# Kernel tuning notes

Measured on AMD Instinct MI355X. Metric: run time of the kernel, lower is better.

The kernel has to match this reference:

```python
import jax, jax.numpy as jnp
import numpy as np

N_NODES = 100000
N_EDGES = 1600000
D_IN = 128
D_H = 128
NUM_GRAPHS = 128


def setup_inputs() -> dict:
    key = jax.random.key(0)
    ks = jax.random.split(key, 16)
    x = jax.random.normal(ks[0], (N_NODES, D_IN), dtype=jnp.float32)
    edge_index = jax.random.randint(ks[1], (2, N_EDGES), 0, N_NODES, dtype=jnp.int64)
    batch_index = jnp.sort(jax.random.randint(ks[2], (N_NODES,), 0, NUM_GRAPHS, dtype=jnp.int64))
    s = 0.05
    W1 = s * jax.random.normal(ks[3], (D_IN, D_H), dtype=jnp.float32)
    b1 = jnp.zeros((D_H,), jnp.float32)
    W2 = s * jax.random.normal(ks[4], (D_H, D_H), dtype=jnp.float32)
    b2 = jnp.zeros((D_H,), jnp.float32)
    W3 = s * jax.random.normal(ks[5], (D_H, D_H), dtype=jnp.float32)
    b3 = jnp.zeros((D_H,), jnp.float32)
    W4 = s * jax.random.normal(ks[6], (D_H, D_H), dtype=jnp.float32)
    b4 = jnp.zeros((D_H,), jnp.float32)
    Wl = s * jax.random.normal(ks[7], (2 * D_H, 1), dtype=jnp.float32)
    bl = jnp.zeros((1,), jnp.float32)
    return {"x": x, "edge_index": edge_index, "batch_index": batch_index,
            "W1": W1, "b1": b1, "W2": W2, "b2": b2, "W3": W3, "b3": b3,
            "W4": W4, "b4": b4, "Wl": Wl, "bl": bl}


def _gcn_prep(edge_index, n_nodes):
    # add self-loops, symmetric normalization D^-1/2 (A+I) D^-1/2
    loops = jnp.arange(n_nodes, dtype=edge_index.dtype)
    row = jnp.concatenate([edge_index[0], loops])  # source
    col = jnp.concatenate([edge_index[1], loops])  # target
    deg = jax.ops.segment_sum(jnp.ones_like(col, dtype=jnp.float32), col,
                              num_segments=n_nodes)
    dinv = jnp.where(deg > 0, jax.lax.rsqrt(jnp.maximum(deg, 1.0)), 0.0)
    norm = dinv[row] * dinv[col]  # [E+N]
    return row, col, norm


def _gcn(h, W, b, row, col, norm, n_nodes):
    h = h @ W                                   # [N, H]
    msg = h[row] * norm[:, None]                # gather + scale
    return jax.ops.segment_sum(msg, col, num_segments=n_nodes) + b


def reference(x, edge_index, batch_index, W1, b1, W2, b2, W3, b3, W4, b4, Wl, bl):
    n = x.shape[0]
    row, col, norm = _gcn_prep(edge_index, n)
    h = jnp.tanh(_gcn(x, W1, b1, row, col, norm, n))
    h = jnp.tanh(_gcn(h, W2, b2, row, col, norm, n))
    h = jnp.tanh(_gcn(h, W3, b3, row, col, norm, n))
    h = jnp.tanh(_gcn(h, W4, b4, row, col, norm, n))
    # global max / mean pool per graph
    cnt = jax.ops.segment_sum(jnp.ones((n,), jnp.float32), batch_index,
                              num_segments=NUM_GRAPHS)
    mx = jax.ops.segment_max(h, batch_index, num_segments=NUM_GRAPHS)
    mx = jnp.where(cnt[:, None] > 0, mx, 0.0)
    sm = jax.ops.segment_sum(h, batch_index, num_segments=NUM_GRAPHS)
    mn = sm / jnp.maximum(cnt, 1.0)[:, None]
    pooled = jnp.concatenate([mx, mn], axis=1)  # [G, 2H]
    return pooled @ Wl + bl                     # [G, 1]
```

## Files before the change

### kernel.cpp

```cpp
#include <hip/hip_runtime.h>
#include <hip/hip_bf16.h>
#include <math.h>

#define PSPLIT 8
#define BSH 8
#define NBMAX 512
#define CHUNK 8192
#define AST 40

typedef float v4f __attribute__((ext_vector_type(4)));
typedef float v2f __attribute__((ext_vector_type(2)));
typedef unsigned int v4u __attribute__((ext_vector_type(4)));
typedef unsigned int v2u __attribute__((ext_vector_type(2)));
typedef __attribute__((ext_vector_type(8))) short bf8;
typedef __attribute__((ext_vector_type(4))) float f4;
typedef unsigned short u16;
typedef unsigned int u32;

static inline size_t align_up(size_t x, size_t a){ return (x + a - 1) & ~(a - 1); }

__device__ inline void bf_split(float v, u16& hi, u16& lo){
  __hip_bfloat16 h = __float2bfloat16(v);
  float hf = __bfloat162float(h);
  __hip_bfloat16 l = __float2bfloat16(v - hf);
  hi = *(u16*)&h; lo = *(u16*)&l;
}

__device__ inline void fmixlo(float& a, u32 p){
  asm("v_fma_mix_f32 %0, %1, 1.0, %0 op_sel:[0,0,0] op_sel_hi:[1,0,0]" : "+v"(a) : "v"(p));
}
__device__ inline void fmixhi(float& a, u32 p){
  asm("v_fma_mix_f32 %0, %1, 1.0, %0 op_sel:[1,0,0] op_sel_hi:[1,0,0]" : "+v"(a) : "v"(p));
}

__device__ inline float tanh_fast(float x){
  float u = __builtin_amdgcn_exp2f(x * 2.8853900817779268f);
  float q = __builtin_amdgcn_rcpf(u + 1.0f);
  return fmaf(-2.0f, q, 1.0f);
}


__global__ __launch_bounds__(256) void k_bhist(const int* __restrict__ col, int* __restrict__ bcnt,
                                               int E, int NB,
                                               const int* __restrict__ batch, int* __restrict__ gstart,
                                               int n, int G){
  extern __shared__ int lh[];
  for (int i = threadIdx.x; i < NB; i += 256) lh[i] = 0;
  __syncthreads();
  for (int e = blockIdx.x * 256 + threadIdx.x; e < E; e += gridDim.x * 256)
    atomicAdd(&lh[col[e] >> BSH], 1);
  __syncthreads();
  for (int i = threadIdx.x; i < NB; i += 256){
    int v = lh[i];
    if (v) atomicAdd(&bcnt[i], v);
  }
  for (int i = blockIdx.x * 256 + threadIdx.x; i < n; i += gridDim.x * 256){
    int cb = batch[i];
    if (i == 0){ for (int g = 0; g <= cb; ++g) gstart[g] = 0; }
    else { int pb = batch[i - 1]; for (int g = pb + 1; g <= cb; ++g) gstart[g] = i; }
    if (i == n - 1){ for (int g = cb + 1; g <= G; ++g) gstart[g] = n; }
  }
}

__global__ void k_bscan(const int* __restrict__ bcnt, int* __restrict__ boff, int NB, int E,
                        int* __restrict__ rp, int N){
  __shared__ int sd[256];
  int t = threadIdx.x;
  int c[16]; int s = 0;
  const int PT = (NB + 255) / 256;
  for (int j = 0; j < PT; ++j){ int i = t * PT + j; c[j] = (i < NB) ? bcnt[i] : 0; s += c[j]; }
  sd[t] = s; __syncthreads();
  for (int off = 1; off < 256; off <<= 1){
    int v = sd[t];
    if (t >= off) v += sd[t - off];
    __syncthreads(); sd[t] = v; __syncthreads();
  }
  int run = sd[t] - s;
  for (int j = 0; j < PT; ++j){ int i = t * PT + j; if (i < NB) boff[i] = run; run += c[j]; }
  if (t == 255){ boff[NB] = run; rp[N] = E; }
}

__global__ __launch_bounds__(256) void k_bscat(const int* __restrict__ ei, const int* __restrict__ boff,
                                               int* __restrict__ bfill, unsigned* __restrict__ tmp,
                                               int E, int NB){
  __shared__ int lh[NBMAX], loff[NBMAX], gb[NBMAX], lfil[NBMAX];
  __shared__ int sd[256];
  __shared__ int sumA;
  __shared__ u32 stg[CHUNK];
  int t = threadIdx.x;
  const int* col = ei + E;
  int c0 = blockIdx.x * CHUNK;
  int c1 = c0 + CHUNK; if (c1 > E) c1 = E;

  for (int i = t; i < NBMAX; i += 256){ lh[i] = 0; lfil[i] = 0; }
  __syncthreads();
  for (int e = c0 + t; e < c1; e += 256)
    atomicAdd(&lh[col[e] >> BSH], 1);
  __syncthreads();
  sd[t] = lh[t]; __syncthreads();
  for (int off = 1; off < 256; off <<= 1){
    int v = sd[t];
    if (t >= off) v += sd[t - off];
    __syncthreads(); sd[t] = v; __syncthreads();
  }
  loff[t] = sd[t] - lh[t];
  if (t == 255) sumA = sd[255];
  __syncthreads();
  int lb = lh[256 + t];
  sd[t] = lb; __syncthreads();
  for (int off = 1; off < 256; off <<= 1){
    int v = sd[t];
    if (t >= off) v += sd[t - off];
    __syncthreads(); sd[t] = v; __syncthreads();
  }
  loff[256 + t] = sumA + sd[t] - lb;
  for (int i = t; i < NB; i += 256){
    int c = lh[i];
    gb[i] = c ? (boff[i] + atomicAdd(&bfill[i * 16], c)) : 0;
  }
  __syncthreads();
  for (int e = c0 + t; e < c1; e += 256){
    int d = col[e], s = ei[e];
    int b = d >> BSH;
    int p = atomicAdd(&lfil[b], 1);
    stg[loff[b] + p] = (unsigned)s | ((unsigned)(d & 255) << 17);
  }
  __syncthreads();
  int wv = t >> 6, lane = t & 63;
  for (int b = wv; b < NB; b += 4){
    int len = lh[b];
    if (!len) continue;
    int base = gb[b], lo = loff[b];
    for (int j = lane; j < len; j += 64) tmp[base + j] = stg[lo + j];
  }
}

__global__ __launch_bounds__(256) void k_bfin(const unsigned* __restrict__ tmp, const int* __restrict__ boff,
                                              int* __restrict__ ssrc, int* __restrict__ rp,
                                              float* __restrict__ dinv, int N){
  int b = blockIdx.x;
  int d0 = b << BSH;
  int lim = N - d0; if (lim > 256) lim = 256;
  __shared__ int dcnt[256], dexc[256], lfill[256];
  int t = threadIdx.x;
  dcnt[t] = 0; lfill[t] = 0;
  __syncthreads();
  int lo = boff[b], hi = boff[b + 1];
  for (int i = lo + t; i < hi; i += 256) atomicAdd(&dcnt[tmp[i] >> 17], 1);
  __syncthreads();
  int cme = dcnt[t];
  dexc[t] = cme; __syncthreads();
  for (int off = 1; off < 256; off <<= 1){
    int v = dexc[t];
    if (t >= off) v += dexc[t - off];
    __syncthreads(); dexc[t] = v; __syncthreads();
  }
  int excl = dexc[t] - cme;
  __syncthreads();
  dexc[t] = excl;
  if (t < lim){
    int d = d0 + t;
    rp[d] = lo + excl;
    double dd = (double)(cme + 1);
    dinv[d] = (float)(1.0 / sqrt(dd));
  }
  __syncthreads();
  for (int i = lo + t; i < hi; i += 256){
    unsigned r = tmp[i];
    int l = r >> 17;
    int pos = dexc[l] + atomicAdd(&lfill[l], 1);
    ssrc[lo + pos] = (int)(r & 0x1FFFFu);
  }
}


__global__ __launch_bounds__(256) void k_cvtw(const float* __restrict__ w0, const float* __restrict__ w1,
                                              const float* __restrict__ w2, const float* __restrict__ w3,
                                              u16* __restrict__ wth, u16* __restrict__ wtl){
  int id = blockIdx.x * 256 + threadIdx.x;
  if (id >= 4 * 16384) return;
  int l = id >> 14, rem = id & 16383, k = rem >> 7, nn = rem & 127;
  const float* Wsrc = (l == 0) ? w0 : (l == 1) ? w1 : (l == 2) ? w2 : w3;
  float v = Wsrc[k * 128 + nn];
  u16 hi, lo; bf_split(v, hi, lo);
  wth[(l << 14) + nn * 128 + k] = hi;
  wtl[(l << 14) + nn * 128 + k] = lo;
}


__global__ __launch_bounds__(256, 4) void k_gemm(const float* __restrict__ A,
                                                 const u16* __restrict__ wth, const u16* __restrict__ wtl,
                                                 const float* __restrict__ dinv,
                                                 u16* __restrict__ C, int n, int packed){
  __shared__ u16 Ah[128 * AST], Al[128 * AST], Wh[128 * AST], Wl[128 * AST];
  int t = threadIdx.x;
  int r0 = blockIdx.x * 128;
  int wv = t >> 6, lane = t & 63;
  int q = lane >> 4, ln = lane & 15;

  int srow = t >> 1;
  int shalf = (t & 1) * 16;
  int grow = r0 + srow; if (grow > n - 1) grow = n - 1;
  const float* ga = A + (size_t)grow * 128 + shalf;
  const u16* gwh = wth + srow * 128 + shalf;
  const u16* gwl = wtl + srow * 128 + shalf;

  f4 acc[2][8];
  #pragma unroll
  for (int mt = 0; mt < 2; ++mt)
    #pragma unroll
    for (int nt = 0; nt < 8; ++nt) acc[mt][nt] = (f4)(0.f);

  for (int c = 0; c < 4; ++c){
    __syncthreads();
    {
      u16* ah = &Ah[srow * AST + shalf];
      u16* al = &Al[srow * AST + shalf];
      if (packed){
        const v4u* gp = (const v4u*)(ga + c * 32);
        #pragma unroll
        for (int i = 0; i < 4; ++i){
          v4u v = gp[i];
          ushort4 hv = {(u16)(v.x >> 16), (u16)(v.y >> 16), (u16)(v.z >> 16), (u16)(v.w >> 16)};
          ushort4 lv = {(u16)v.x, (u16)v.y, (u16)v.z, (u16)v.w};
          *(ushort4*)&ah[i * 4] = hv;
          *(ushort4*)&al[i * 4] = lv;
        }
      } else {
        const float4* gp = (const float4*)(ga + c * 32);
        #pragma unroll
        for (int i = 0; i < 4; ++i){
          float4 v = gp[i];
          u16 h0,h1,h2,h3,l0,l1,l2,l3;
          bf_split(v.x, h0, l0); bf_split(v.y, h1, l1);
          bf_split(v.z, h2, l2); bf_split(v.w, h3, l3);
          ushort4 hv = {h0,h1,h2,h3}, lv = {l0,l1,l2,l3};
          *(ushort4*)&ah[i * 4] = hv;
          *(ushort4*)&al[i * 4] = lv;
        }
      }
    }
    {
      const u16* ph = gwh + c * 32;
      const u16* pl = gwl + c * 32;
      bf8 h0 = *(const bf8*)ph, h1 = *(const bf8*)(ph + 8);
      bf8 l0 = *(const bf8*)pl, l1 = *(const bf8*)(pl + 8);
      *(bf8*)&Wh[srow * AST + shalf] = h0; *(bf8*)&Wh[srow * AST + shalf + 8] = h1;
      *(bf8*)&Wl[srow * AST + shalf] = l0; *(bf8*)&Wl[srow * AST + shalf + 8] = l1;
    }
    __syncthreads();

    bf8 afh[2], afl[2];
    #pragma unroll
    for (int mt = 0; mt < 2; ++mt){
      int row = wv * 32 + mt * 16 + ln;
      afh[mt] = *(const bf8*)&Ah[row * AST + q * 8];
      afl[mt] = *(const bf8*)&Al[row * AST + q * 8];
    }
    #pragma unroll
    for (int nt = 0; nt < 8; ++nt){
      int wn = nt * 16 + ln;
      bf8 wfh = *(const bf8*)&Wh[wn * AST + q * 8];
      bf8 wfl = *(const bf8*)&Wl[wn * AST + q * 8];
      #pragma unroll
      for (int mt = 0; mt < 2; ++mt){
        acc[mt][nt] = __builtin_amdgcn_mfma_f32_16x16x32_bf16(afh[mt], wfh, acc[mt][nt], 0, 0, 0);
        acc[mt][nt] = __builtin_amdgcn_mfma_f32_16x16x32_bf16(afl[mt], wfh, acc[mt][nt], 0, 0, 0);
        acc[mt][nt] = __builtin_amdgcn_mfma_f32_16x16x32_bf16(afh[mt], wfl, acc[mt][nt], 0, 0, 0);
      }
    }
  }

  #pragma unroll
  for (int mt = 0; mt < 2; ++mt){
    int base_m = r0 + wv * 32 + mt * 16 + q * 4;
    float dv[4];
    #pragma unroll
    for (int reg = 0; reg < 4; ++reg){
      int row = base_m + reg;
      dv[reg] = (row < n) ? dinv[row] : 0.f;
    }
    #pragma unroll
    for (int nt = 0; nt < 8; ++nt){
      #pragma unroll
      for (int reg = 0; reg < 4; ++reg){
        int row = base_m + reg;
        if (row < n){
          _Float16 hv = (_Float16)(acc[mt][nt][reg] * dv[reg]);
          C[(size_t)row * 128 + nt * 16 + ln] = *(u16*)&hv;
        }
      }
    }
  }
}


__global__ __launch_bounds__(256) void k_agg(const u16* __restrict__ hwp, const int* __restrict__ rp,
                                             const int* __restrict__ ssrc,
                                             const float* __restrict__ dinv, const float* __restrict__ bias,
                                             float* __restrict__ hout, int n, int pack){
  int node = blockIdx.x * 4 + (threadIdx.x >> 6);
  node = __builtin_amdgcn_readfirstlane(node);
  if (node >= n) return;
  int lane = threadIdx.x & 63;
  const u32* hw32 = (const u32*)hwp;

  int e0 = rp[node], e1 = rp[node + 1];
  float a0 = 0.f, a1 = 0.f;
  int e = e0;
  while (e + 16 <= e1){
    u32 p[16];
    #pragma unroll
    for (int i = 0; i < 16; ++i){
      int s = ssrc[e + i];
      p[i] = hw32[(size_t)s * 64 + lane];
    }
    #pragma unroll
    for (int i = 0; i < 16; ++i){ fmixlo(a0, p[i]); fmixhi(a1, p[i]); }
    e += 16;
  }
  while (e + 4 <= e1){
    u32 p[4];
    #pragma unroll
    for (int i = 0; i < 4; ++i){
      int s = ssrc[e + i];
      p[i] = hw32[(size_t)s * 64 + lane];
    }
    #pragma unroll
    for (int i = 0; i < 4; ++i){ fmixlo(a0, p[i]); fmixhi(a1, p[i]); }
    e += 4;
  }
  while (e < e1){
    int s = ssrc[e];
    u32 p = hw32[(size_t)s * 64 + lane];
    fmixlo(a0, p); fmixhi(a1, p);
    ++e;
  }
  {
    u32 p = hw32[(size_t)node * 64 + lane];
    fmixlo(a0, p); fmixhi(a1, p);
  }
  float di = dinv[node];
  v2f bv = *(const v2f*)(bias + lane * 2);
  float r0 = tanh_fast(fmaf(a0, di, bv.x));
  float r1 = tanh_fast(fmaf(a1, di, bv.y));
  if (pack){
    u16 h0, h1, l0, l1;
    bf_split(r0, h0, l0); bf_split(r1, h1, l1);
    v2u pv;
    pv.x = ((u32)h0 << 16) | l0;
    pv.y = ((u32)h1 << 16) | l1;
    __builtin_nontemporal_store(pv, (v2u*)((u32*)hout + (size_t)node * 128 + lane * 2));
  } else {
    v2f rr; rr.x = r0; rr.y = r1;
    __builtin_nontemporal_store(rr, (v2f*)(hout + (size_t)node * 128 + lane * 2));
  }
}


__global__ __launch_bounds__(256) void k_pool1(const float* __restrict__ h, const int* __restrict__ gstart,
                                               float* __restrict__ pmx, float* __restrict__ psm){
  int g = blockIdx.x >> 3, s = blockIdx.x & (PSPLIT - 1);
  int t = threadIdx.x;
  int fq = t & 31;
  int rw = t >> 5;
  int i0 = gstart[g], i1 = gstart[g + 1];
  int len = i1 - i0;
  int chunk = (len + PSPLIT - 1) / PSPLIT;
  int a = i0 + s * chunk;
  int b = a + chunk; if (b > i1) b = i1;

  const v4f* hv = (const v4f*)h;
  v4f mx = (v4f)(-INFINITY), sm = (v4f)(0.f);
  for (int i = a + rw; i < b; i += 8){
    v4f v = hv[(size_t)i * 32 + fq];
    mx.x = fmaxf(mx.x, v.x); mx.y = fmaxf(mx.y, v.y);
    mx.z = fmaxf(mx.z, v.z); mx.w = fmaxf(mx.w, v.w);
    sm += v;
  }
  __shared__ v4f smx[8][32], ssm[8][32];
  smx[rw][fq] = mx; ssm[rw][fq] = sm;
  __syncthreads();
  if (rw == 0){
    #pragma unroll
    for (int r2 = 1; r2 < 8; ++r2){
      v4f m2 = smx[r2][fq], s2 = ssm[r2][fq];
      mx.x = fmaxf(mx.x, m2.x); mx.y = fmaxf(mx.y, m2.y);
      mx.z = fmaxf(mx.z, m2.z); mx.w = fmaxf(mx.w, m2.w);
      sm += s2;
    }
    ((v4f*)pmx)[(size_t)blockIdx.x * 32 + fq] = mx;
    ((v4f*)psm)[(size_t)blockIdx.x * 32 + fq] = sm;
  }
}

__global__ __launch_bounds__(128) void k_head(const float* __restrict__ pmx, const float* __restrict__ psm,
                                              const int* __restrict__ gstart,
                                              const float* __restrict__ Wl, const float* __restrict__ bl,
                                              float* __restrict__ out){
  int g = blockIdx.x, f = threadIdx.x;
  float mx = -INFINITY, sm = 0.f;
  #pragma unroll
  for (int s = 0; s < PSPLIT; ++s){
    mx = fmaxf(mx, pmx[((size_t)g * PSPLIT + s) * 128 + f]);
    sm += psm[((size_t)g * PSPLIT + s) * 128 + f];
  }
  int cnt = gstart[g + 1] - gstart[g];
  if (cnt <= 0) mx = 0.f;
  float mn = sm / (float)(cnt > 0 ? cnt : 1);
  float contrib = mx * Wl[f] + mn * Wl[128 + f];
  for (int o = 32; o > 0; o >>= 1) contrib += __shfl_down(contrib, o);
  __shared__ float sred[2];
  if ((f & 63) == 0) sred[f >> 6] = contrib;
  __syncthreads();
  if (f == 0) out[g] = sred[0] + sred[1] + bl[0];
}


extern "C" void kernel_launch(void* const* d_in, const int* in_sizes, int n_in,
                              void* d_out, int out_size, void* d_ws, size_t ws_size,
                              hipStream_t stream){
  const float* x     = (const float*)d_in[0];
  const int*   ei    = (const int*)d_in[1];
  const int*   batch = (const int*)d_in[2];
  const float* W[4]  = {(const float*)d_in[3], (const float*)d_in[5], (const float*)d_in[7], (const float*)d_in[9]};
  const float* B[4]  = {(const float*)d_in[4], (const float*)d_in[6], (const float*)d_in[8], (const float*)d_in[10]};
  const float* Wl    = (const float*)d_in[11];
  const float* bl    = (const float*)d_in[12];
  float* out = (float*)d_out;

  int N = in_sizes[0] / 128;
  int E = in_sizes[1] / 2;
  int G = out_size;
  int NB = (N + 255) >> BSH;

  char* ws = (char*)d_ws;
  size_t off = 0;
  auto alloc = [&](size_t bytes) -> void* {
    void* p = ws + off; off = align_up(off + bytes, 256); return p;
  };
  float* dinv  = (float*)alloc((size_t)N * 4);
  int*   rp    = (int*)  alloc((size_t)(N + 1) * 4);
  int*   bcnt  = (int*)  alloc((size_t)(NB + 1) * 4);
  int*   boff  = (int*)  alloc((size_t)(NB + 1) * 4);
  int*   bfill = (int*)  alloc((size_t)NB * 16 * 4);
  int*   gst   = (int*)  alloc((size_t)(G + 1) * 4);
  int*   ssrc  = (int*)  alloc((size_t)E * 4);
  u16*   wth   = (u16*)  alloc((size_t)4 * 16384 * 2);
  u16*   wtl   = (u16*)  alloc((size_t)4 * 16384 * 2);
  float* pmx   = (float*)alloc((size_t)G * PSPLIT * 128 * 4);
  float* psm   = (float*)alloc((size_t)G * PSPLIT * 128 * 4);
  u16*   hw    = (u16*)  alloc((size_t)N * 128 * 2);
  float* h     = (float*)alloc((size_t)N * 128 * 4);
  unsigned* tmp = (unsigned*)hw;

  hipMemsetAsync(bcnt, 0, (size_t)(NB + 1) * 4, stream);
  hipMemsetAsync(bfill, 0, (size_t)NB * 16 * 4, stream);

  k_cvtw <<<256, 256, 0, stream>>>(W[0], W[1], W[2], W[3], wth, wtl);
  k_bhist<<<128, 256, NB * 4, stream>>>(ei + E, bcnt, E, NB, batch, gst, N, G);
  k_bscan<<<1, 256, 0, stream>>>(bcnt, boff, NB, E, rp, N);
  k_bscat<<<(E + CHUNK - 1) / CHUNK, 256, 0, stream>>>(ei, boff, bfill, tmp, E, NB);
  k_bfin <<<NB, 256, 0, stream>>>(tmp, boff, ssrc, rp, dinv, N);

  int gemmG = (N + 127) / 128;
  int aggG  = (N + 3) / 4;
  const float* hin = x;
  for (int l = 0; l < 4; ++l){
    k_gemm<<<gemmG, 256, 0, stream>>>(hin, wth + (l << 14), wtl + (l << 14), dinv, hw, N, l > 0);
    k_agg <<<aggG, 256, 0, stream>>>(hw, rp, ssrc, dinv, B[l], h, N, l < 3);
    hin = h;
  }
  k_pool1<<<G * PSPLIT, 256, 0, stream>>>(h, gst, pmx, psm);
  k_head <<<G, 128, 0, stream>>>(pmx, psm, gst, Wl, bl, out);
}
```

Baseline: 556.3 us.

## Store hidden activations as fp16 and use fp16 MFMA with split weights

```diff
diff --git a/kernel.cpp b/kernel.cpp
--- a/kernel.cpp
+++ b/kernel.cpp
@@ -13,6 +13,7 @@
 typedef unsigned int v4u __attribute__((ext_vector_type(4)));
 typedef unsigned int v2u __attribute__((ext_vector_type(2)));
 typedef __attribute__((ext_vector_type(8))) short bf8;
+typedef _Float16 h8 __attribute__((ext_vector_type(8)));
 typedef __attribute__((ext_vector_type(4))) float f4;
 typedef unsigned short u16;
 typedef unsigned int u32;
@@ -32,6 +33,9 @@
 __device__ inline void fmixhi(float& a, u32 p){
   asm("v_fma_mix_f32 %0, %1, 1.0, %0 op_sel:[1,0,0] op_sel_hi:[1,0,0]" : "+v"(a) : "v"(p));
 }
+
+__device__ inline float f16lo(u32 p){ u16 q = (u16)p; return (float)*(_Float16*)&q; }
+__device__ inline float f16hi(u32 p){ u16 q = (u16)(p >> 16); return (float)*(_Float16*)&q; }
 
 __device__ inline float tanh_fast(float x){
   float u = __builtin_amdgcn_exp2f(x * 2.8853900817779268f);
@@ -176,15 +180,22 @@
 
 __global__ __launch_bounds__(256) void k_cvtw(const float* __restrict__ w0, const float* __restrict__ w1,
                                               const float* __restrict__ w2, const float* __restrict__ w3,
-                                              u16* __restrict__ wth, u16* __restrict__ wtl){
+                                              u16* __restrict__ wth, u16* __restrict__ wtl,
+                                              u16* __restrict__ fth, u16* __restrict__ ftl){
   int id = blockIdx.x * 256 + threadIdx.x;
   if (id >= 4 * 16384) return;
   int l = id >> 14, rem = id & 16383, k = rem >> 7, nn = rem & 127;
   const float* Wsrc = (l == 0) ? w0 : (l == 1) ? w1 : (l == 2) ? w2 : w3;
   float v = Wsrc[k * 128 + nn];
   u16 hi, lo; bf_split(v, hi, lo);
-  wth[(l << 14) + nn * 128 + k] = hi;
-  wtl[(l << 14) + nn * 128 + k] = lo;
+  int idx = (l << 14) + nn * 128 + k;
+  wth[idx] = hi;
+  wtl[idx] = lo;
+  _Float16 fh = (_Float16)v;
+  float fr = v - (float)fh;
+  _Float16 fl = (_Float16)fr;
+  fth[idx] = *(u16*)&fh;
+  ftl[idx] = *(u16*)&fl;
 }
 
 
@@ -202,6 +213,7 @@
   int shalf = (t & 1) * 16;
   int grow = r0 + srow; if (grow > n - 1) grow = n - 1;
   const float* ga = A + (size_t)grow * 128 + shalf;
+  const u32* gap = (const u32*)A + (size_t)grow * 64 + (shalf >> 1);
   const u16* gwh = wth + srow * 128 + shalf;
   const u16* gwl = wtl + srow * 128 + shalf;
 
@@ -213,31 +225,29 @@
 
   for (int c = 0; c < 4; ++c){
     __syncthreads();
-    {
+    if (packed){
+      const v4u* gp = (const v4u*)(gap + c * 16);
+      v4u v0 = gp[0], v1 = gp[1];
+      u16* af = &Ah[srow * AST + shalf];
+      ushort4 a0 = {(u16)v0.x, (u16)(v0.x >> 16), (u16)v0.y, (u16)(v0.y >> 16)};
+      ushort4 a1 = {(u16)v0.z, (u16)(v0.z >> 16), (u16)v0.w, (u16)(v0.w >> 16)};
+      ushort4 a2 = {(u16)v1.x, (u16)(v1.x >> 16), (u16)v1.y, (u16)(v1.y >> 16)};
+      ushort4 a3 = {(u16)v1.z, (u16)(v1.z >> 16), (u16)v1.w, (u16)(v1.w >> 16)};
+      *(ushort4*)&af[0]  = a0; *(ushort4*)&af[4]  = a1;
+      *(ushort4*)&af[8]  = a2; *(ushort4*)&af[12] = a3;
+    } else {
       u16* ah = &Ah[srow * AST + shalf];
       u16* al = &Al[srow * AST + shalf];
-      if (packed){
-        const v4u* gp = (const v4u*)(ga + c * 32);
-        #pragma unroll
-        for (int i = 0; i < 4; ++i){
-          v4u v = gp[i];
-          ushort4 hv = {(u16)(v.x >> 16), (u16)(v.y >> 16), (u16)(v.z >> 16), (u16)(v.w >> 16)};
-          ushort4 lv = {(u16)v.x, (u16)v.y, (u16)v.z, (u16)v.w};
-          *(ushort4*)&ah[i * 4] = hv;
-          *(ushort4*)&al[i * 4] = lv;
-        }
-      } else {
-        const float4* gp = (const float4*)(ga + c * 32);
-        #pragma unroll
-        for (int i = 0; i < 4; ++i){
-          float4 v = gp[i];
-          u16 h0,h1,h2,h3,l0,l1,l2,l3;
-          bf_split(v.x, h0, l0); bf_split(v.y, h1, l1);
-          bf_split(v.z, h2, l2); bf_split(v.w, h3, l3);
-          ushort4 hv = {h0,h1,h2,h3}, lv = {l0,l1,l2,l3};
-          *(ushort4*)&ah[i * 4] = hv;
-          *(ushort4*)&al[i * 4] = lv;
-        }
+      const float4* gp = (const float4*)(ga + c * 32);
+      #pragma unroll
+      for (int i = 0; i < 4; ++i){
+        float4 v = gp[i];
+        u16 h0,h1,h2,h3,l0,l1,l2,l3;
+        bf_split(v.x, h0, l0); bf_split(v.y, h1, l1);
+        bf_split(v.z, h2, l2); bf_split(v.w, h3, l3);
+        ushort4 hv = {h0,h1,h2,h3}, lv = {l0,l1,l2,l3};
+        *(ushort4*)&ah[i * 4] = hv;
+        *(ushort4*)&al[i * 4] = lv;
       }
     }
     {
@@ -250,23 +260,43 @@
     }
     __syncthreads();
 
-    bf8 afh[2], afl[2];
-    #pragma unroll
-    for (int mt = 0; mt < 2; ++mt){
-      int row = wv * 32 + mt * 16 + ln;
-      afh[mt] = *(const bf8*)&Ah[row * AST + q * 8];
-      afl[mt] = *(const bf8*)&Al[row * AST + q * 8];
-    }
-    #pragma unroll
-    for (int nt = 0; nt < 8; ++nt){
-      int wn = nt * 16 + ln;
-      bf8 wfh = *(const bf8*)&Wh[wn * AST + q * 8];
-      bf8 wfl = *(const bf8*)&Wl[wn * AST + q * 8];
+    if (packed){
+      h8 af[2];
       #pragma unroll
       for (int mt = 0; mt < 2; ++mt){
-        acc[mt][nt] = __builtin_amdgcn_mfma_f32_16x16x32_bf16(afh[mt], wfh, acc[mt][nt], 0, 0, 0);
-        acc[mt][nt] = __builtin_amdgcn_mfma_f32_16x16x32_bf16(afl[mt], wfh, acc[mt][nt], 0, 0, 0);
-        acc[mt][nt] = __builtin_amdgcn_mfma_f32_16x16x32_bf16(afh[mt], wfl, acc[mt][nt], 0, 0, 0);
+        int row = wv * 32 + mt * 16 + ln;
+        af[mt] = *(const h8*)&Ah[row * AST + q * 8];
+      }
+      #pragma unroll
+      for (int nt = 0; nt < 8; ++nt){
+        int wn = nt * 16 + ln;
+        h8 wfh = *(const h8*)&Wh[wn * AST + q * 8];
+        h8 wfl = *(const h8*)&Wl[wn * AST + q * 8];
+        #pragma unroll
+        for (int mt = 0; mt < 2; ++mt){
+          acc[mt][nt] = __builtin_amdgcn_mfma_f32_16x16x32_f16(af[mt], wfh, acc[mt][nt], 0, 0, 0);
+          acc[mt][nt] = __builtin_amdgcn_mfma_f32_16x16x32_f16(af[mt], wfl, acc[mt][nt], 0, 0, 0);
+        }
+      }
+    } else {
+      bf8 afh[2], afl[2];
+      #pragma unroll
+      for (int mt = 0; mt < 2; ++mt){
+        int row = wv * 32 + mt * 16 + ln;
+        afh[mt] = *(const bf8*)&Ah[row * AST + q * 8];
+        afl[mt] = *(const bf8*)&Al[row * AST + q * 8];
+      }
+      #pragma unroll
+      for (int nt = 0; nt < 8; ++nt){
+        int wn = nt * 16 + ln;
+        bf8 wfh = *(const bf8*)&Wh[wn * AST + q * 8];
+        bf8 wfl = *(const bf8*)&Wl[wn * AST + q * 8];
+        #pragma unroll
+        for (int mt = 0; mt < 2; ++mt){
+          acc[mt][nt] = __builtin_amdgcn_mfma_f32_16x16x32_bf16(afh[mt], wfh, acc[mt][nt], 0, 0, 0);
+          acc[mt][nt] = __builtin_amdgcn_mfma_f32_16x16x32_bf16(afl[mt], wfh, acc[mt][nt], 0, 0, 0);
+          acc[mt][nt] = __builtin_amdgcn_mfma_f32_16x16x32_bf16(afh[mt], wfl, acc[mt][nt], 0, 0, 0);
+        }
       }
     }
   }
@@ -298,7 +328,7 @@
 __global__ __launch_bounds__(256) void k_agg(const u16* __restrict__ hwp, const int* __restrict__ rp,
                                              const int* __restrict__ ssrc,
                                              const float* __restrict__ dinv, const float* __restrict__ bias,
-                                             float* __restrict__ hout, int n, int pack){
+                                             u32* __restrict__ hout, int n){
   int node = blockIdx.x * 4 + (threadIdx.x >> 6);
   node = __builtin_amdgcn_readfirstlane(node);
   if (node >= n) return;
@@ -344,21 +374,13 @@
   v2f bv = *(const v2f*)(bias + lane * 2);
   float r0 = tanh_fast(fmaf(a0, di, bv.x));
   float r1 = tanh_fast(fmaf(a1, di, bv.y));
-  if (pack){
-    u16 h0, h1, l0, l1;
-    bf_split(r0, h0, l0); bf_split(r1, h1, l1);
-    v2u pv;
-    pv.x = ((u32)h0 << 16) | l0;
-    pv.y = ((u32)h1 << 16) | l1;
-    __builtin_nontemporal_store(pv, (v2u*)((u32*)hout + (size_t)node * 128 + lane * 2));
-  } else {
-    v2f rr; rr.x = r0; rr.y = r1;
-    __builtin_nontemporal_store(rr, (v2f*)(hout + (size_t)node * 128 + lane * 2));
-  }
-}
-
-
-__global__ __launch_bounds__(256) void k_pool1(const float* __restrict__ h, const int* __restrict__ gstart,
+  _Float16 f0 = (_Float16)r0, f1 = (_Float16)r1;
+  u32 pv = ((u32)(*(u16*)&f1) << 16) | (u32)(*(u16*)&f0);
+  __builtin_nontemporal_store(pv, hout + (size_t)node * 64 + lane);
+}
+
+
+__global__ __launch_bounds__(256) void k_pool1(const u32* __restrict__ h, const int* __restrict__ gstart,
                                                float* __restrict__ pmx, float* __restrict__ psm){
   int g = blockIdx.x >> 3, s = blockIdx.x & (PSPLIT - 1);
   int t = threadIdx.x;
@@ -370,13 +392,14 @@
   int a = i0 + s * chunk;
   int b = a + chunk; if (b > i1) b = i1;
 
-  const v4f* hv = (const v4f*)h;
+  const v2u* hv = (const v2u*)h;
   v4f mx = (v4f)(-INFINITY), sm = (v4f)(0.f);
   for (int i = a + rw; i < b; i += 8){
-    v4f v = hv[(size_t)i * 32 + fq];
-    mx.x = fmaxf(mx.x, v.x); mx.y = fmaxf(mx.y, v.y);
-    mx.z = fmaxf(mx.z, v.z); mx.w = fmaxf(mx.w, v.w);
-    sm += v;
+    v2u p = hv[(size_t)i * 32 + fq];
+    float x0 = f16lo(p.x), x1 = f16hi(p.x), x2 = f16lo(p.y), x3 = f16hi(p.y);
+    mx.x = fmaxf(mx.x, x0); mx.y = fmaxf(mx.y, x1);
+    mx.z = fmaxf(mx.z, x2); mx.w = fmaxf(mx.w, x3);
+    sm.x += x0; sm.y += x1; sm.z += x2; sm.w += x3;
   }
   __shared__ v4f smx[8][32], ssm[8][32];
   smx[rw][fq] = mx; ssm[rw][fq] = sm;
@@ -448,16 +471,18 @@
   int*   ssrc  = (int*)  alloc((size_t)E * 4);
   u16*   wth   = (u16*)  alloc((size_t)4 * 16384 * 2);
   u16*   wtl   = (u16*)  alloc((size_t)4 * 16384 * 2);
+  u16*   fth   = (u16*)  alloc((size_t)4 * 16384 * 2);
+  u16*   ftl   = (u16*)  alloc((size_t)4 * 16384 * 2);
   float* pmx   = (float*)alloc((size_t)G * PSPLIT * 128 * 4);
   float* psm   = (float*)alloc((size_t)G * PSPLIT * 128 * 4);
   u16*   hw    = (u16*)  alloc((size_t)N * 128 * 2);
-  float* h     = (float*)alloc((size_t)N * 128 * 4);
+  u32*   h     = (u32*)  alloc((size_t)N * 64 * 4);
   unsigned* tmp = (unsigned*)hw;
 
   hipMemsetAsync(bcnt, 0, (size_t)(NB + 1) * 4, stream);
   hipMemsetAsync(bfill, 0, (size_t)NB * 16 * 4, stream);
 
-  k_cvtw <<<256, 256, 0, stream>>>(W[0], W[1], W[2], W[3], wth, wtl);
+  k_cvtw <<<256, 256, 0, stream>>>(W[0], W[1], W[2], W[3], wth, wtl, fth, ftl);
   k_bhist<<<128, 256, NB * 4, stream>>>(ei + E, bcnt, E, NB, batch, gst, N, G);
   k_bscan<<<1, 256, 0, stream>>>(bcnt, boff, NB, E, rp, N);
   k_bscat<<<(E + CHUNK - 1) / CHUNK, 256, 0, stream>>>(ei, boff, bfill, tmp, E, NB);
@@ -467,9 +492,11 @@
   int aggG  = (N + 3) / 4;
   const float* hin = x;
   for (int l = 0; l < 4; ++l){
-    k_gemm<<<gemmG, 256, 0, stream>>>(hin, wth + (l << 14), wtl + (l << 14), dinv, hw, N, l > 0);
-    k_agg <<<aggG, 256, 0, stream>>>(hw, rp, ssrc, dinv, B[l], h, N, l < 3);
-    hin = h;
+    const u16* wh = (l == 0) ? (wth + (l << 14)) : (fth + (l << 14));
+    const u16* wl = (l == 0) ? (wtl + (l << 14)) : (ftl + (l << 14));
+    k_gemm<<<gemmG, 256, 0, stream>>>(hin, wh, wl, dinv, hw, N, l > 0);
+    k_agg <<<aggG, 256, 0, stream>>>(hw, rp, ssrc, dinv, B[l], h, N);
+    hin = (const float*)h;
   }
   k_pool1<<<G * PSPLIT, 256, 0, stream>>>(h, gst, pmx, psm);
   k_head <<<G, 128, 0, stream>>>(pmx, psm, gst, Wl, bl, out);
```

Result: slower. 591.9 us (+6.4%).
